# Kernel tuning notes

Hardware: AMD Instinct MI355X
Metric: run time of the kernel (lower is better)

## Reference

```python
import jax, jax.numpy as jnp
import numpy as np

C = 64
HIMG = 256
WIMG = 256
N = HIMG * WIMG
E = 8 * N
HEADS = 4
DHEAD = C // HEADS
NMOD = 9   # 9 GraphAttentionModules (c1_1..c3_3)
NLAY = 3   # layers per module
NSTACK = 2 # RBS1, RBS2
NBLK = 4   # resblocks per stack


def setup_inputs() -> dict:
    key = jax.random.key(0)
    ks = jax.random.split(key, 12)
    s = 0.05
    x = jax.random.normal(ks[0], (1, C, HIMG, WIMG), dtype=jnp.float32)
    edge_index = jax.random.randint(ks[1], (2, E), 0, N, dtype=jnp.int32)
    gat_Wl = jax.random.normal(ks[2], (NMOD, NLAY, C, C), dtype=jnp.float32) * s
    gat_Wr = jax.random.normal(ks[3], (NMOD, NLAY, C, C), dtype=jnp.float32) * s
    gat_att = jax.random.normal(ks[4], (NMOD, NLAY, HEADS, DHEAD), dtype=jnp.float32) * s
    gat_b = jax.random.normal(ks[5], (NMOD, NLAY, C), dtype=jnp.float32) * s
    cc_w = jax.random.normal(ks[6], (3, C, 3 * C), dtype=jnp.float32) * s
    cc_b = jax.random.normal(ks[7], (3, C), dtype=jnp.float32) * s
    rb_w = jax.random.normal(ks[8], (NSTACK, NBLK, 2, C, C, 3, 3), dtype=jnp.float32) * s
    rb_b = jax.random.normal(ks[9], (NSTACK, NBLK, 2, C), dtype=jnp.float32) * s
    rb_a = jnp.full((NSTACK, NBLK), 0.25, dtype=jnp.float32)  # PReLU init
    return dict(x=x, edge_index=edge_index, gat_Wl=gat_Wl, gat_Wr=gat_Wr,
                gat_att=gat_att, gat_b=gat_b, cc_w=cc_w, cc_b=cc_b,
                rb_w=rb_w, rb_b=rb_b, rb_a=rb_a)


def _gatv2(x, src, dst, Wl, Wr, att, b):
    # x: [N,C]; GATv2Conv (PyG): xl = lin_l(x) (source msgs), xr = lin_r(x) (target)
    xl = (x @ Wl).reshape(-1, HEADS, DHEAD)
    xr = (x @ Wr).reshape(-1, HEADS, DHEAD)
    xj = xl[src]                               # [E,H,D] source
    xi = xr[dst]                               # [E,H,D] target
    e = jax.nn.leaky_relu(xi + xj, 0.2)        # [E,H,D]
    logits = jnp.einsum('ehd,hd->eh', e, att)  # [E,H]
    m = jax.ops.segment_max(logits, dst, num_segments=N)
    m = jnp.where(jnp.isfinite(m), m, 0.0)
    ex = jnp.exp(logits - m[dst])
    den = jax.ops.segment_sum(ex, dst, num_segments=N)
    alpha = ex / (den[dst] + 1e-16)            # edge softmax per target node
    out = jax.ops.segment_sum(xj * alpha[..., None], dst, num_segments=N)
    return out.reshape(-1, C) + b


def _gam(xn, src, dst, m, gat_Wl, gat_Wr, gat_att, gat_b):
    # GraphAttentionModule: 3 GAT layers, each followed by ELU
    for l in range(NLAY):
        xn = jax.nn.elu(_gatv2(xn, src, dst, gat_Wl[m, l], gat_Wr[m, l],
                               gat_att[m, l], gat_b[m, l]))
    return xn


def _to_nodes(img):   # [1,C,H,W] -> [N,C]
    return img[0].transpose(1, 2, 0).reshape(N, C)


def _to_img(xn):      # [N,C] -> [1,C,H,W]
    return xn.reshape(HIMG, WIMG, C).transpose(2, 0, 1)[None]


def _conv3(x, w, b):
    y = jax.lax.conv_general_dilated(x, w, (1, 1), 'SAME',
                                     dimension_numbers=('NCHW', 'OIHW', 'NCHW'))
    return y + b[None, :, None, None]


def _resblocks(x, w, b, a):
    # stack of 4 ResBlocks: conv3 -> PReLU -> conv3, res_scale=1
    for i in range(NBLK):
        h = _conv3(x, w[i, 0], b[i, 0])
        h = jnp.where(h >= 0, h, a[i] * h)  # PReLU (single shared param)
        h = _conv3(h, w[i, 1], b[i, 1])
        x = x + h
    return x


def _stage(img, midx, ci, src, dst, gat_Wl, gat_Wr, gat_att, gat_b, cc_w, cc_b):
    xn = _to_nodes(img)
    branches = [_to_img(_gam(xn, src, dst, m, gat_Wl, gat_Wr, gat_att, gat_b))
                for m in midx]
    cat = jnp.concatenate(branches, axis=1)            # [1,3C,H,W]
    out = jnp.einsum('oc,bchw->bohw', cc_w[ci], cat) + cc_b[ci][None, :, None, None]
    return out + img


def reference(x, edge_index, gat_Wl, gat_Wr, gat_att, gat_b, cc_w, cc_b,
              rb_w, rb_b, rb_a):
    src, dst = edge_index[0], edge_index[1]
    out = _stage(x, (0, 1, 2), 0, src, dst, gat_Wl, gat_Wr, gat_att, gat_b, cc_w, cc_b)
    out = _resblocks(out, rb_w[0], rb_b[0], rb_a[0])
    out = _stage(out, (3, 4, 5), 1, src, dst, gat_Wl, gat_Wr, gat_att, gat_b, cc_w, cc_b)
    out = _resblocks(out, rb_w[1], rb_b[1], rb_a[1])
    out = _stage(out, (6, 7, 8), 2, src, dst, gat_Wl, gat_Wr, gat_att, gat_b, cc_w, cc_b)
    return out
```

## Files before the change

kernel.cpp:

```cpp
#include <hip/hip_runtime.h>
#include <hip/hip_bf16.h>
#include <math.h>

#define N_NODES 65536
#define HW      65536
#define NE      524288
#define NC      (N_NODES * 64)

typedef __bf16 bf16x8 __attribute__((ext_vector_type(8)));
typedef float  f32x4  __attribute__((ext_vector_type(4)));
typedef float  f32x2  __attribute__((ext_vector_type(2)));
typedef int    i32x4  __attribute__((ext_vector_type(4)));
typedef unsigned int uint2v __attribute__((ext_vector_type(2)));

static __device__ __forceinline__ f32x4 mfma16(bf16x8 a, bf16x8 b, f32x4 c) {
    return __builtin_amdgcn_mfma_f32_16x16x32_bf16(a, b, c, 0, 0, 0);
}

static __device__ __forceinline__ unsigned short f2bs(float f) {
    return __builtin_bit_cast(unsigned short, __float2bfloat16(f));
}

__global__ void k_hist(const int* __restrict__ dstA, int* __restrict__ cnt) {
    int e = blockIdx.x * 256 + threadIdx.x;
    if (e < NE) atomicAdd(&cnt[dstA[e]], 1);
}

__global__ void k_scan(const int* __restrict__ cnt, int* __restrict__ off) {
    __shared__ int sums[1024];
    int t = threadIdx.x;
    int base = t * 64;
    int s = 0;
    for (int i = 0; i < 64; ++i) s += cnt[base + i];
    sums[t] = s;
    __syncthreads();
    for (int d = 1; d < 1024; d <<= 1) {
        int v = (t >= d) ? sums[t - d] : 0;
        __syncthreads();
        sums[t] += v;
        __syncthreads();
    }
    int run = sums[t] - s;
    for (int i = 0; i < 64; ++i) { off[base + i] = run; run += cnt[base + i]; }
    if (t == 1023) off[N_NODES] = run;
}

__global__ void k_fill(const int* __restrict__ srcA, const int* __restrict__ dstA,
                       int* __restrict__ cur, int* __restrict__ csr) {
    int e = blockIdx.x * 256 + threadIdx.x;
    if (e < NE) {
        int p = atomicAdd(&cur[dstA[e]], 1);
        csr[p] = srcA[e];
    }
}

__global__ void k_cvpack(const float* __restrict__ w, __hip_bfloat16* __restrict__ d) {
    int idx = blockIdx.x * 256 + threadIdx.x;
    if (idx >= 589824) return;
    int j = idx & 7, lane = (idx >> 3) & 63, r = idx >> 9;
    int kk = r & 1; r >>= 1;
    int nt = r & 3; r >>= 2;
    int tap = r % 9, cv = r / 9;
    int co = nt * 16 + (lane & 15);
    int ci = kk * 32 + (lane >> 4) * 8 + j;
    d[idx] = __float2bfloat16(w[((cv * 64 + co) * 64 + ci) * 9 + tap]);
}

__global__ void k_mmpack(const float* __restrict__ Wl, const float* __restrict__ Wr,
                         __hip_bfloat16* __restrict__ d) {
    int idx = blockIdx.x * 256 + threadIdx.x;
    if (idx >= 221184) return;
    int j = idx & 7, lane = (idx >> 3) & 63, r = idx >> 9;
    int kk = r & 1; r >>= 1;
    int nt = r & 3; r >>= 2;
    int side = r & 1, lay = r >> 1;
    int co = nt * 16 + (lane & 15);
    int ci = kk * 32 + (lane >> 4) * 8 + j;
    const float* W = side ? Wr : Wl;
    d[idx] = __float2bfloat16(W[lay * 4096 + ci * 64 + co]);
}

__global__ void k_ccpack(const float* __restrict__ w, __hip_bfloat16* __restrict__ d) {
    int idx = blockIdx.x * 256 + threadIdx.x;
    if (idx >= 36864) return;
    int j = idx & 7;
    int u = idx >> 3;
    int lane = u & 63;
    int f = (u >> 6) & 7;
    int sb = u >> 9;
    int kk = f & 1, nt = f >> 1;
    int br = sb % 3, st = sb / 3;
    int k = br * 64 + kk * 32 + (lane >> 4) * 8 + j;
    int co = nt * 16 + (lane & 15);
    d[idx] = __float2bfloat16(w[st * 12288 + co * 192 + k]);
}

__global__ void k_init(const float* __restrict__ img, float* __restrict__ xn,
                       __hip_bfloat16* __restrict__ xb) {
    __shared__ float tile[64][65];
    int nb = blockIdx.x * 64;
    for (int idx = threadIdx.x; idx < 4096; idx += 256) {
        int c = idx >> 6, n = idx & 63;
        tile[c][n] = img[c * HW + nb + n];
    }
    __syncthreads();
    for (int idx = threadIdx.x; idx < 4096; idx += 256) {
        int n = idx >> 6, c = idx & 63;
        float v = tile[c][n];
        xn[(nb + n) * 64 + c] = v;
        xb[(nb + n) * 64 + c] = __float2bfloat16(v);
    }
}

static __device__ __forceinline__ void mm_phase32(char* smem, int t,
        const __hip_bfloat16* __restrict__ pwm, unsigned char* __restrict__ xlo,
        __hip_bfloat16* __restrict__ xrb, int n0) {
    i32x4* la = (i32x4*)smem;
    int lane = t & 63, side = t >> 6;
    const i32x4* wpt = (const i32x4*)pwm + side * 512 + lane;
    f32x4 acc[2][4];
#pragma unroll
    for (int mi = 0; mi < 2; ++mi)
#pragma unroll
        for (int nt = 0; nt < 4; ++nt) acc[mi][nt] = (f32x4)0.0f;
    bf16x8 b[4][2];
#pragma unroll
    for (int nt = 0; nt < 4; ++nt)
#pragma unroll
        for (int kk = 0; kk < 2; ++kk)
            b[nt][kk] = __builtin_bit_cast(bf16x8, wpt[(nt * 2 + kk) * 64]);
#pragma unroll
    for (int mi = 0; mi < 2; ++mi) {
        int row = mi * 16 + (lane & 15);
#pragma unroll
        for (int kk = 0; kk < 2; ++kk) {
            bf16x8 a = __builtin_bit_cast(bf16x8,
                la[row * 8 + (((kk << 2) | (lane >> 4)) ^ (row & 7))]);
#pragma unroll
            for (int nt = 0; nt < 4; ++nt)
                acc[mi][nt] = mfma16(a, b[nt][kk], acc[mi][nt]);
        }
    }
    __syncthreads();
    unsigned short* ls = (unsigned short*)smem;
    if (side == 0) {
#pragma unroll
        for (int mi = 0; mi < 2; ++mi)
#pragma unroll
            for (int nt = 0; nt < 4; ++nt) {
                int co = nt * 16 + (lane & 15);
#pragma unroll
                for (int r = 0; r < 4; ++r) {
                    int row = mi * 16 + (lane >> 4) * 4 + r;
                    ls[row * 68 + co] = f2bs(acc[mi][nt][r]);
                }
            }
    } else {
#pragma unroll
        for (int mi = 0; mi < 2; ++mi)
#pragma unroll
            for (int nt = 0; nt < 4; ++nt) {
                int co = nt * 16 + (lane & 15);
#pragma unroll
                for (int r = 0; r < 4; ++r) {
                    int node = n0 + mi * 16 + (lane >> 4) * 4 + r;
                    xrb[(size_t)node * 64 + co] = __float2bfloat16(acc[mi][nt][r]);
                }
            }
    }
    __syncthreads();
    for (int u = t; u < 256; u += 128) {
        int node = u >> 3, oct = u & 7;
        const unsigned short* p = ls + node * 68 + oct * 8;
        uint2v w0 = *(const uint2v*)p;
        uint2v w1 = *(const uint2v*)(p + 4);
        float f0 = __builtin_bit_cast(float, w0[0] << 16);
        float f1 = __builtin_bit_cast(float, w0[0] & 0xffff0000u);
        float f2 = __builtin_bit_cast(float, w0[1] << 16);
        float f3 = __builtin_bit_cast(float, w0[1] & 0xffff0000u);
        float f4 = __builtin_bit_cast(float, w1[0] << 16);
        float f5 = __builtin_bit_cast(float, w1[0] & 0xffff0000u);
        float f6 = __builtin_bit_cast(float, w1[1] << 16);
        float f7 = __builtin_bit_cast(float, w1[1] & 0xffff0000u);
        int v0 = 0, v1 = 0;
        v0 = __builtin_amdgcn_cvt_pk_fp8_f32(f0, f1, v0, false);
        v0 = __builtin_amdgcn_cvt_pk_fp8_f32(f2, f3, v0, true);
        v1 = __builtin_amdgcn_cvt_pk_fp8_f32(f4, f5, v1, false);
        v1 = __builtin_amdgcn_cvt_pk_fp8_f32(f6, f7, v1, true);
        uint2v o;
        o[0] = (unsigned)v0;
        o[1] = (unsigned)v1;
        *(uint2v*)(xlo + (size_t)(n0 + node) * 64 + oct * 8) = o;
    }
}

static __device__ __forceinline__ uint2v gat_node(
        const unsigned char* __restrict__ xl8, const __hip_bfloat16* __restrict__ xrb,
        const int* __restrict__ csr, const int* __restrict__ csr_c, int cbase, int cc,
        int n, int e0, int e1, int c4, f32x2 a01, f32x2 a23, f32x4 b4) {
    uint2v xw = *(const uint2v*)(xrb + (size_t)n * 64 + c4);
    f32x2 xi01, xi23;
    xi01[0] = __builtin_bit_cast(float, xw[0] << 16);
    xi01[1] = __builtin_bit_cast(float, xw[0] & 0xffff0000u);
    xi23[0] = __builtin_bit_cast(float, xw[1] << 16);
    xi23[1] = __builtin_bit_cast(float, xw[1] & 0xffff0000u);
    float s = 0.f;
    f32x2 acc01 = {0.f, 0.f}, acc23 = {0.f, 0.f};
    int rounds = (e1 - e0 + 1) >> 1;
    int e = e0;
    for (int i = 0; i < rounds; ++i, e += 2) {
        bool aB = (e + 1) < e1;
        int eB = aB ? e + 1 : e;
        int rA = e - cbase, rB = eB - cbase;
        int sA = (rA < cc) ? csr_c[rA] : csr[e];
        int sB = (rB < cc) ? csr_c[rB] : csr[eB];
        unsigned int wA = *(const unsigned int*)(xl8 + (size_t)sA * 64 + c4);
        unsigned int wB = *(const unsigned int*)(xl8 + (size_t)sB * 64 + c4);
        f32x2 xjA01 = __builtin_amdgcn_cvt_pk_f32_fp8((int)wA, false);
        f32x2 xjA23 = __builtin_amdgcn_cvt_pk_f32_fp8((int)wA, true);
        f32x2 xjB01 = __builtin_amdgcn_cvt_pk_f32_fp8((int)wB, false);
        f32x2 xjB23 = __builtin_amdgcn_cvt_pk_f32_fp8((int)wB, true);
        f32x2 vA01 = xi01 + xjA01;
        f32x2 vA23 = xi23 + xjA23;
        vA01 = __builtin_elementwise_max(vA01, vA01 * 0.2f);
        vA23 = __builtin_elementwise_max(vA23, vA23 * 0.2f);
        f32x2 pA2 = vA01 * a01 + vA23 * a23;
        float pA = pA2[0] + pA2[1];
        f32x2 vB01 = xi01 + xjB01;
        f32x2 vB23 = xi23 + xjB23;
        vB01 = __builtin_elementwise_max(vB01, vB01 * 0.2f);
        vB23 = __builtin_elementwise_max(vB23, vB23 * 0.2f);
        f32x2 pB2 = vB01 * a01 + vB23 * a23;
        float pB = pB2[0] + pB2[1];
        pA += __shfl_xor(pA, 1);
        pA += __shfl_xor(pA, 2);
        pB += __shfl_xor(pB, 1);
        pB += __shfl_xor(pB, 2);
        float exA = exp2f(fmaxf(pA, -100.f));
        float exB = exp2f(fmaxf(pB, -100.f));
        exB = aB ? exB : 0.f;
        s += exA + exB;
        acc01 = acc01 + exA * xjA01 + exB * xjB01;
        acc23 = acc23 + exA * xjA23 + exB * xjB23;
    }
    float inv = __builtin_amdgcn_rcpf(s + 1e-16f);
    float v0 = fmaf(acc01[0], inv, b4[0]);
    float v1 = fmaf(acc01[1], inv, b4[1]);
    float v2 = fmaf(acc23[0], inv, b4[2]);
    float v3 = fmaf(acc23[1], inv, b4[3]);
    v0 = v0 > 0.f ? v0 : __expf(v0) - 1.f;
    v1 = v1 > 0.f ? v1 : __expf(v1) - 1.f;
    v2 = v2 > 0.f ? v2 : __expf(v2) - 1.f;
    v3 = v3 > 0.f ? v3 : __expf(v3) - 1.f;
    uint2v o;
    o[0] = (unsigned)f2bs(v0) | ((unsigned)f2bs(v1) << 16);
    o[1] = (unsigned)f2bs(v2) | ((unsigned)f2bs(v3) << 16);
    return o;
}

__global__ __launch_bounds__(128) void k_mm3(const __hip_bfloat16* __restrict__ Xb,
        const __hip_bfloat16* __restrict__ pw, unsigned char* __restrict__ XL8,
        __hip_bfloat16* __restrict__ XRb) {
    __shared__ i32x4 smem4[272];
    char* smem = (char*)smem4;
    i32x4* la = (i32x4*)smem;
    int t = threadIdx.x;
    int m = blockIdx.x >> 11;
    int n0 = (blockIdx.x & 2047) << 5;
    const i32x4* Xg = (const i32x4*)Xb + n0 * 8;
    for (int idx = t; idx < 256; idx += 128) {
        int r = idx >> 3, c = idx & 7;
        la[r * 8 + (c ^ (r & 7))] = Xg[idx];
    }
    __syncthreads();
    mm_phase32(smem, t, pw + m * 24576, XL8 + (size_t)m * NC,
               XRb + (size_t)m * NC, n0);
}

__global__ __launch_bounds__(128) void k_fuse(
        const unsigned char* __restrict__ XL8in, unsigned char* __restrict__ XL8out,
        __hip_bfloat16* __restrict__ XRb, const float* __restrict__ gatt,
        const float* __restrict__ gb, const __hip_bfloat16* __restrict__ pw,
        const int* __restrict__ off, const int* __restrict__ csr) {
    __shared__ i32x4 smem4[272];
    __shared__ int csr_c[384];
    char* smem = (char*)smem4;
    int t = threadIdx.x;
    int p = blockIdx.x;
    int vi = (p & 7) * 768 + (p >> 3);
    int m = vi >> 11;
    int n0 = (vi & 2047) << 5;
    const unsigned char* xl8 = XL8in + (size_t)m * NC;
    unsigned char* xlo = XL8out + (size_t)m * NC;
    __hip_bfloat16* xrb = XRb + (size_t)m * NC;
    int cbase = off[n0];
    int cc = min(off[n0 + 32] - cbase, 384);
    for (int i = t; i < cc; i += 128) csr_c[i] = csr[cbase + i];
    __syncthreads();
    int g16 = t >> 4;
    int c4 = (t & 15) << 2;
    const float* at = gatt + m * 192;
    const float* bb = gb + m * 192;
    const float LOG2E = 1.44269504089f;
    f32x4 a4 = *(const f32x4*)(at + c4);
    f32x2 a01 = {a4[0] * LOG2E, a4[1] * LOG2E};
    f32x2 a23 = {a4[2] * LOG2E, a4[3] * LOG2E};
    f32x4 b4 = *(const f32x4*)(bb + c4);
    uint2v* lau = (uint2v*)smem;
    int cchunk = c4 >> 3, half = (c4 >> 2) & 1;
    for (int nn = 0; nn < 4; ++nn) {
        int r = g16 * 4 + nn;
        int n = n0 + r;
        uint2v o = gat_node(xl8, xrb, csr, csr_c, cbase, cc, n,
                            off[n], off[n + 1], c4, a01, a23, b4);
        lau[(r * 8 + (cchunk ^ (r & 7))) * 2 + half] = o;
    }
    __syncthreads();
    mm_phase32(smem, t, pw + m * 24576, xlo, xrb, n0);
}

__global__ __launch_bounds__(256) void k_gatfin(const unsigned char* __restrict__ XL8,
        const __hip_bfloat16* __restrict__ XRb, const float* __restrict__ gatt,
        const float* __restrict__ gb, const int* __restrict__ off,
        const int* __restrict__ csr, __hip_bfloat16* __restrict__ brs) {
    __shared__ int csr_c[320];
    int t = threadIdx.x, lane = t & 63;
    int p = blockIdx.x;
    int vi = (p & 7) * 768 + (p >> 3);
    int m = vi >> 11;
    int nblk = (vi & 2047) * 32;
    const unsigned char* xl8 = XL8 + (size_t)m * NC;
    const __hip_bfloat16* xrb = XRb + (size_t)m * NC;
    __hip_bfloat16* outb = brs + (size_t)m * NC;
    int cbase = off[nblk];
    int cc = min(off[nblk + 32] - cbase, 320);
    for (int i = t; i < cc; i += 256) csr_c[i] = csr[cbase + i];
    __syncthreads();
    int g = (lane >> 4) & 3;
    int c4 = (lane & 15) << 2;
    const float* at = gatt + m * 192;
    const float* bb = gb + m * 192;
    const float LOG2E = 1.44269504089f;
    f32x4 a4 = *(const f32x4*)(at + c4);
    f32x2 a01 = {a4[0] * LOG2E, a4[1] * LOG2E};
    f32x2 a23 = {a4[2] * LOG2E, a4[3] * LOG2E};
    f32x4 b4 = *(const f32x4*)(bb + c4);
    int base = nblk + ((t >> 6) << 3) + g * 2;
#pragma unroll
    for (int nn = 0; nn < 2; ++nn) {
        int n = base + nn;
        uint2v o = gat_node(xl8, xrb, csr, csr_c, cbase, cc, n,
                            off[n], off[n + 1], c4, a01, a23, b4);
        *(uint2v*)(outb + (size_t)n * 64 + c4) = o;
    }
}

__global__ __launch_bounds__(256) void k_cc2(const __hip_bfloat16* __restrict__ b0,
        const __hip_bfloat16* __restrict__ b1, const __hip_bfloat16* __restrict__ b2,
        const __hip_bfloat16* __restrict__ pw, const float* __restrict__ bias,
        const float* __restrict__ resin, float* __restrict__ imgout,
        __hip_bfloat16* __restrict__ outb) {
    __shared__ i32x4 la[128 * 8];
    int t = threadIdx.x, lane = t & 63, wid = t >> 6;
    int n0 = blockIdx.x * 128;
    const __hip_bfloat16* brs[3] = {b0, b1, b2};
    const i32x4* wp4 = (const i32x4*)pw;
    f32x4 acc[2][4];
#pragma unroll
    for (int mi = 0; mi < 2; ++mi)
#pragma unroll
        for (int nt = 0; nt < 4; ++nt) acc[mi][nt] = (f32x4)0.0f;
#pragma unroll
    for (int br = 0; br < 3; ++br) {
        __syncthreads();
        const i32x4* Bg = (const i32x4*)brs[br] + n0 * 8;
        for (int idx = t; idx < 1024; idx += 256) {
            int r = idx >> 3, c = idx & 7;
            la[r * 8 + (c ^ (r & 7))] = Bg[idx];
        }
        __syncthreads();
        bf16x8 bf[4][2];
#pragma unroll
        for (int nt = 0; nt < 4; ++nt)
#pragma unroll
            for (int kk = 0; kk < 2; ++kk)
                bf[nt][kk] = __builtin_bit_cast(bf16x8,
                    wp4[(br * 8 + nt * 2 + kk) * 64 + lane]);
#pragma unroll
        for (int mi = 0; mi < 2; ++mi) {
            int row = wid * 32 + mi * 16 + (lane & 15);
#pragma unroll
            for (int kk = 0; kk < 2; ++kk) {
                bf16x8 a = __builtin_bit_cast(bf16x8,
                    la[row * 8 + (((kk << 2) | (lane >> 4)) ^ (row & 7))]);
#pragma unroll
                for (int nt = 0; nt < 4; ++nt)
                    acc[mi][nt] = mfma16(a, bf[nt][kk], acc[mi][nt]);
            }
        }
    }
#pragma unroll
    for (int mi = 0; mi < 2; ++mi)
#pragma unroll
        for (int nt = 0; nt < 4; ++nt) {
            int co = nt * 16 + (lane & 15);
            float bv = bias[co];
#pragma unroll
            for (int r = 0; r < 4; ++r) {
                int node = n0 + wid * 32 + mi * 16 + (lane >> 4) * 4 + r;
                float v = acc[mi][nt][r] + bv + resin[node * 64 + co];
                imgout[node * 64 + co] = v;
                outb[node * 64 + co] = __float2bfloat16(v);
            }
        }
}

__global__ __launch_bounds__(256) void k_ccfin(const __hip_bfloat16* __restrict__ b0,
        const __hip_bfloat16* __restrict__ b1, const __hip_bfloat16* __restrict__ b2,
        const __hip_bfloat16* __restrict__ pw, const float* __restrict__ bias,
        const float* __restrict__ resin, float* __restrict__ outp) {
    __shared__ i32x4 la[128 * 8];
    __shared__ float tt[64][132];
    int t = threadIdx.x, lane = t & 63, wid = t >> 6;
    int n0 = blockIdx.x * 128;
    const __hip_bfloat16* brs[3] = {b0, b1, b2};
    const i32x4* wp4 = (const i32x4*)pw;
    f32x4 acc[2][4];
#pragma unroll
    for (int mi = 0; mi < 2; ++mi)
#pragma unroll
        for (int nt = 0; nt < 4; ++nt) acc[mi][nt] = (f32x4)0.0f;
#pragma unroll
    for (int br = 0; br < 3; ++br) {
        __syncthreads();
        const i32x4* Bg = (const i32x4*)brs[br] + n0 * 8;
        for (int idx = t; idx < 1024; idx += 256) {
            int r = idx >> 3, c = idx & 7;
            la[r * 8 + (c ^ (r & 7))] = Bg[idx];
        }
        __syncthreads();
        bf16x8 bf[4][2];
#pragma unroll
        for (int nt = 0; nt < 4; ++nt)
#pragma unroll
            for (int kk = 0; kk < 2; ++kk)
                bf[nt][kk] = __builtin_bit_cast(bf16x8,
                    wp4[(br * 8 + nt * 2 + kk) * 64 + lane]);
#pragma unroll
        for (int mi = 0; mi < 2; ++mi) {
            int row = wid * 32 + mi * 16 + (lane & 15);
#pragma unroll
            for (int kk = 0; kk < 2; ++kk) {
                bf16x8 a = __builtin_bit_cast(bf16x8,
                    la[row * 8 + (((kk << 2) | (lane >> 4)) ^ (row & 7))]);
#pragma unroll
                for (int nt = 0; nt < 4; ++nt)
                    acc[mi][nt] = mfma16(a, bf[nt][kk], acc[mi][nt]);
            }
        }
    }
#pragma unroll
    for (int mi = 0; mi < 2; ++mi)
#pragma unroll
        for (int nt = 0; nt < 4; ++nt) {
            int co = nt * 16 + (lane & 15);
            float bv = bias[co];
#pragma unroll
            for (int r = 0; r < 4; ++r) {
                int nl = wid * 32 + mi * 16 + (lane >> 4) * 4 + r;
                tt[co][nl] = acc[mi][nt][r] + bv + resin[(n0 + nl) * 64 + co];
            }
        }
    __syncthreads();
    for (int u = t; u < 2048; u += 256) {
        int row = u >> 5;
        int col = (u & 31) * 4;
        f32x4 v = *(const f32x4*)&tt[row][col];
        *(f32x4*)(outp + row * HW + n0 + col) = v;
    }
}

template <int MODE>
__global__ __launch_bounds__(256) void k_conv(const __hip_bfloat16* __restrict__ inb,
        const __hip_bfloat16* __restrict__ wp, const float* __restrict__ bias,
        const float* __restrict__ pa, float* __restrict__ img,
        __hip_bfloat16* __restrict__ outb) {
    __shared__ i32x4 la[2][130 * 8];
    int t = threadIdx.x, lane = t & 63, wid = t >> 6;
    int y = blockIdx.x >> 1, x0 = (blockIdx.x & 1) << 7;
    f32x4 acc[2][4];
#pragma unroll
    for (int mi = 0; mi < 2; ++mi)
#pragma unroll
        for (int nt = 0; nt < 4; ++nt) acc[mi][nt] = (f32x4)0.0f;
    const i32x4* ing = (const i32x4*)inb;
    auto stage = [&](int dy, int buf) {
        int sy = y + dy - 1;
        bool rowok = (sy >= 0) && (sy < 256);
        for (int idx = t; idx < 1040; idx += 256) {
            int r = idx >> 3, c = idx & 7;
            int sx = x0 - 1 + r;
            i32x4 v = (i32x4)0;
            if (rowok && sx >= 0 && sx < 256) v = ing[(sy * 256 + sx) * 8 + c];
            la[buf][r * 8 + (c ^ (r & 7))] = v;
        }
    };
    stage(0, 0);
    __syncthreads();
#pragma unroll
    for (int dy = 0; dy < 3; ++dy) {
        if (dy < 2) stage(dy + 1, (dy + 1) & 1);
        const i32x4* lb = la[dy & 1];
#pragma unroll
        for (int dx = 0; dx < 3; ++dx) {
            const i32x4* wpt = (const i32x4*)wp + (dy * 3 + dx) * 512 + lane;
            bf16x8 b[4][2];
#pragma unroll
            for (int nt = 0; nt < 4; ++nt)
#pragma unroll
                for (int kk = 0; kk < 2; ++kk)
                    b[nt][kk] = __builtin_bit_cast(bf16x8, wpt[(nt * 2 + kk) * 64]);
#pragma unroll
            for (int mi = 0; mi < 2; ++mi) {
                int row = dx + wid * 32 + mi * 16 + (lane & 15);
#pragma unroll
                for (int kk = 0; kk < 2; ++kk) {
                    bf16x8 a = __builtin_bit_cast(bf16x8,
                        lb[row * 8 + (((kk << 2) | (lane >> 4)) ^ (row & 7))]);
#pragma unroll
                    for (int nt = 0; nt < 4; ++nt)
                        acc[mi][nt] = mfma16(a, b[nt][kk], acc[mi][nt]);
                }
            }
        }
        __syncthreads();
    }
    int pbase = y * 256 + x0 + wid * 32 + (lane >> 4) * 4;
    float aprelu = (MODE == 0) ? pa[0] : 0.f;
#pragma unroll
    for (int mi = 0; mi < 2; ++mi)
#pragma unroll
        for (int nt = 0; nt < 4; ++nt) {
            int co = nt * 16 + (lane & 15);
            float bv = bias[co];
#pragma unroll
            for (int r = 0; r < 4; ++r) {
                int pix = pbase + mi * 16 + r;
                float v = acc[mi][nt][r] + bv;
                if (MODE == 0) {
                    v = v >= 0.f ? v : aprelu * v;
                    outb[pix * 64 + co] = __float2bfloat16(v);
                } else {
                    v += img[pix * 64 + co];
                    img[pix * 64 + co] = v;
                    outb[pix * 64 + co] = __float2bfloat16(v);
                }
            }
        }
}

extern "C" void kernel_launch(void* const* d_in, const int* in_sizes, int n_in,
                              void* d_out, int out_size, void* d_ws, size_t ws_size,
                              hipStream_t stream) {
    const float* x    = (const float*)d_in[0];
    const int*   ei   = (const int*)d_in[1];
    const float* gWl  = (const float*)d_in[2];
    const float* gWr  = (const float*)d_in[3];
    const float* gatt = (const float*)d_in[4];
    const float* gb   = (const float*)d_in[5];
    const float* ccw  = (const float*)d_in[6];
    const float* ccb  = (const float*)d_in[7];
    const float* rbw  = (const float*)d_in[8];
    const float* rbb  = (const float*)d_in[9];
    const float* rba  = (const float*)d_in[10];
    float* outp = (float*)d_out;

    float* wsf = (float*)d_ws;
    float* xn  = wsf;
    float* img = xn + NC;
    __hip_bfloat16* xrb3 = (__hip_bfloat16*)(img + NC);
    unsigned char* xl8p0 = (unsigned char*)(xrb3 + 3 * (size_t)NC);
    unsigned char* xl8p1 = xl8p0 + 3 * (size_t)NC;
    __hip_bfloat16* xb   = (__hip_bfloat16*)(xl8p1 + 3 * (size_t)NC);
    __hip_bfloat16* b0b  = xb + NC;
    __hip_bfloat16* b1b  = b0b + NC;
    __hip_bfloat16* b2b  = b1b + NC;
    __hip_bfloat16* cvb  = b0b;
    __hip_bfloat16* wpkc = b2b + NC;
    __hip_bfloat16* wpkm = wpkc + 589824;
    __hip_bfloat16* ccpk = wpkm + 221184;
    int* ioff = (int*)(ccpk + 36864);
    int* icnt = ioff + (N_NODES + 1);
    int* icur = icnt + N_NODES;
    int* icsr = icur + N_NODES;

    const int* srcA = ei;
    const int* dstA = ei + NE;

    hipMemsetAsync(icnt, 0, N_NODES * sizeof(int), stream);
    k_hist<<<NE / 256, 256, 0, stream>>>(dstA, icnt);
    k_scan<<<1, 1024, 0, stream>>>(icnt, ioff);
    hipMemcpyAsync(icur, ioff, N_NODES * sizeof(int), hipMemcpyDeviceToDevice, stream);
    k_fill<<<NE / 256, 256, 0, stream>>>(srcA, dstA, icur, icsr);
    k_cvpack<<<2304, 256, 0, stream>>>(rbw, wpkc);
    k_mmpack<<<864, 256, 0, stream>>>(gWl, gWr, wpkm);
    k_ccpack<<<144, 256, 0, stream>>>(ccw, ccpk);
    k_init<<<1024, 256, 0, stream>>>(x, xn, xb);

    for (int st = 0; st < 3; ++st) {
        int L = st * 9;
        k_mm3<<<6144, 128, 0, stream>>>(xb, wpkm + (size_t)L * 8192, xl8p0, xrb3);
        k_fuse<<<6144, 128, 0, stream>>>(xl8p0, xl8p1, xrb3,
            gatt + L * 64, gb + L * 64, wpkm + (size_t)(L + 1) * 8192, ioff, icsr);
        k_fuse<<<6144, 128, 0, stream>>>(xl8p1, xl8p0, xrb3,
            gatt + (L + 1) * 64, gb + (L + 1) * 64, wpkm + (size_t)(L + 2) * 8192,
            ioff, icsr);
        k_gatfin<<<6144, 256, 0, stream>>>(xl8p0, xrb3,
            gatt + (L + 2) * 64, gb + (L + 2) * 64, ioff, icsr, b0b);
        const float* resin = (st == 0) ? xn : img;
        if (st == 2) {
            k_ccfin<<<N_NODES / 128, 256, 0, stream>>>(b0b, b1b, b2b,
                ccpk + 2 * 12288, ccb + 128, resin, outp);
        } else {
            k_cc2<<<N_NODES / 128, 256, 0, stream>>>(b0b, b1b, b2b,
                ccpk + st * 12288, ccb + st * 64, resin, img, xb);
            for (int bk = 0; bk < 4; ++bk) {
                int cv = (st * 4 + bk) * 2;
                k_conv<0><<<512, 256, 0, stream>>>(xb, wpkc + (size_t)cv * 36864,
                    rbb + cv * 64, rba + st * 4 + bk, nullptr, cvb);
                k_conv<1><<<512, 256, 0, stream>>>(cvb, wpkc + (size_t)(cv + 1) * 36864,
                    rbb + (cv + 1) * 64, nullptr, img, xb);
            }
        }
    }
}
```

Measured before the change: 0.9996 ms.

## Degree-sort nodes within blocks for GAT balance and halve conv tile width

A new setup kernel sorts the 32 nodes of each block by in-degree. The fused GAT kernels then assign nodes to thread groups in a snake order over that ranking, so each group gets a similar total edge count and the wave waits less on its slowest group. Separately, the 3x3 conv kernel now covers 64 pixels per block instead of 128 (1024 blocks instead of 512), which reduces per-thread accumulators and raises the number of blocks in flight. The cost is more halo reloads in the conv and an extra indirection load per node in the GAT kernels.

Measured after the change: 971.3 us. 2.8% less time.

```diff
diff --git a/kernel.cpp b/kernel.cpp
--- a/kernel.cpp
+++ b/kernel.cpp
@@ -52,6 +52,29 @@
         int p = atomicAdd(&cur[dstA[e]], 1);
         csr[p] = srcA[e];
     }
+}
+
+__global__ void k_bsort(const int* __restrict__ off, int* __restrict__ bperm) {
+    int b = blockIdx.x * 256 + threadIdx.x;
+    if (b >= 2048) return;
+    int base = b * 32;
+    int deg[32], idx[32];
+#pragma unroll
+    for (int i = 0; i < 32; ++i) {
+        deg[i] = off[base + i + 1] - off[base + i];
+        idx[i] = i;
+    }
+    for (int i = 1; i < 32; ++i) {
+        int d = deg[i], x = idx[i], j = i - 1;
+        while (j >= 0 && deg[j] < d) {
+            deg[j + 1] = deg[j];
+            idx[j + 1] = idx[j];
+            --j;
+        }
+        deg[j + 1] = d;
+        idx[j + 1] = x;
+    }
+    for (int i = 0; i < 32; ++i) bperm[base + i] = idx[i];
 }
 
 __global__ void k_cvpack(const float* __restrict__ w, __hip_bfloat16* __restrict__ d) {
@@ -281,7 +304,8 @@
         const unsigned char* __restrict__ XL8in, unsigned char* __restrict__ XL8out,
         __hip_bfloat16* __restrict__ XRb, const float* __restrict__ gatt,
         const float* __restrict__ gb, const __hip_bfloat16* __restrict__ pw,
-        const int* __restrict__ off, const int* __restrict__ csr) {
+        const int* __restrict__ off, const int* __restrict__ csr,
+        const int* __restrict__ bperm) {
     __shared__ i32x4 smem4[272];
     __shared__ int csr_c[384];
     char* smem = (char*)smem4;
@@ -308,8 +332,11 @@
     f32x4 b4 = *(const f32x4*)(bb + c4);
     uint2v* lau = (uint2v*)smem;
     int cchunk = c4 >> 3, half = (c4 >> 2) & 1;
+    const int* bp = bperm + n0;
+#pragma unroll
     for (int nn = 0; nn < 4; ++nn) {
-        int r = g16 * 4 + nn;
+        int rank = (nn & 1) ? (nn * 8 + (7 - g16)) : (nn * 8 + g16);
+        int r = bp[rank];
         int n = n0 + r;
         uint2v o = gat_node(xl8, xrb, csr, csr_c, cbase, cc, n,
                             off[n], off[n + 1], c4, a01, a23, b4);
@@ -322,7 +349,8 @@
 __global__ __launch_bounds__(256) void k_gatfin(const unsigned char* __restrict__ XL8,
         const __hip_bfloat16* __restrict__ XRb, const float* __restrict__ gatt,
         const float* __restrict__ gb, const int* __restrict__ off,
-        const int* __restrict__ csr, __hip_bfloat16* __restrict__ brs) {
+        const int* __restrict__ csr, __hip_bfloat16* __restrict__ brs,
+        const int* __restrict__ bperm) {
     __shared__ int csr_c[320];
     int t = threadIdx.x, lane = t & 63;
     int p = blockIdx.x;
@@ -337,6 +365,7 @@
     for (int i = t; i < cc; i += 256) csr_c[i] = csr[cbase + i];
     __syncthreads();
     int g = (lane >> 4) & 3;
+    int gg = (t >> 6) * 4 + g;
     int c4 = (lane & 15) << 2;
     const float* at = gatt + m * 192;
     const float* bb = gb + m * 192;
@@ -345,10 +374,11 @@
     f32x2 a01 = {a4[0] * LOG2E, a4[1] * LOG2E};
     f32x2 a23 = {a4[2] * LOG2E, a4[3] * LOG2E};
     f32x4 b4 = *(const f32x4*)(bb + c4);
-    int base = nblk + ((t >> 6) << 3) + g * 2;
+    const int* bp = bperm + nblk;
 #pragma unroll
     for (int nn = 0; nn < 2; ++nn) {
-        int n = base + nn;
+        int rank = (nn & 1) ? (16 + (15 - gg)) : gg;
+        int n = nblk + bp[rank];
         uint2v o = gat_node(xl8, xrb, csr, csr_c, cbase, cc, n,
                             off[n], off[n + 1], c4, a01, a23, b4);
         *(uint2v*)(outb + (size_t)n * 64 + c4) = o;
@@ -485,19 +515,17 @@
         const __hip_bfloat16* __restrict__ wp, const float* __restrict__ bias,
         const float* __restrict__ pa, float* __restrict__ img,
         __hip_bfloat16* __restrict__ outb) {
-    __shared__ i32x4 la[2][130 * 8];
+    __shared__ i32x4 la[2][66 * 8];
     int t = threadIdx.x, lane = t & 63, wid = t >> 6;
-    int y = blockIdx.x >> 1, x0 = (blockIdx.x & 1) << 7;
-    f32x4 acc[2][4];
-#pragma unroll
-    for (int mi = 0; mi < 2; ++mi)
-#pragma unroll
-        for (int nt = 0; nt < 4; ++nt) acc[mi][nt] = (f32x4)0.0f;
+    int y = blockIdx.x >> 2, x0 = (blockIdx.x & 3) << 6;
+    f32x4 acc[4];
+#pragma unroll
+    for (int nt = 0; nt < 4; ++nt) acc[nt] = (f32x4)0.0f;
     const i32x4* ing = (const i32x4*)inb;
     auto stage = [&](int dy, int buf) {
         int sy = y + dy - 1;
         bool rowok = (sy >= 0) && (sy < 256);
-        for (int idx = t; idx < 1040; idx += 256) {
+        for (int idx = t; idx < 528; idx += 256) {
             int r = idx >> 3, c = idx & 7;
             int sx = x0 - 1 + r;
             i32x4 v = (i32x4)0;
@@ -520,43 +548,38 @@
 #pragma unroll
                 for (int kk = 0; kk < 2; ++kk)
                     b[nt][kk] = __builtin_bit_cast(bf16x8, wpt[(nt * 2 + kk) * 64]);
-#pragma unroll
-            for (int mi = 0; mi < 2; ++mi) {
-                int row = dx + wid * 32 + mi * 16 + (lane & 15);
-#pragma unroll
-                for (int kk = 0; kk < 2; ++kk) {
-                    bf16x8 a = __builtin_bit_cast(bf16x8,
-                        lb[row * 8 + (((kk << 2) | (lane >> 4)) ^ (row & 7))]);
-#pragma unroll
-                    for (int nt = 0; nt < 4; ++nt)
-                        acc[mi][nt] = mfma16(a, b[nt][kk], acc[mi][nt]);
-                }
+            int row = dx + wid * 16 + (lane & 15);
+#pragma unroll
+            for (int kk = 0; kk < 2; ++kk) {
+                bf16x8 a = __builtin_bit_cast(bf16x8,
+                    lb[row * 8 + (((kk << 2) | (lane >> 4)) ^ (row & 7))]);
+#pragma unroll
+                for (int nt = 0; nt < 4; ++nt)
+                    acc[nt] = mfma16(a, b[nt][kk], acc[nt]);
             }
         }
         __syncthreads();
     }
-    int pbase = y * 256 + x0 + wid * 32 + (lane >> 4) * 4;
+    int pbase = y * 256 + x0 + wid * 16 + (lane >> 4) * 4;
     float aprelu = (MODE == 0) ? pa[0] : 0.f;
 #pragma unroll
-    for (int mi = 0; mi < 2; ++mi)
-#pragma unroll
-        for (int nt = 0; nt < 4; ++nt) {
-            int co = nt * 16 + (lane & 15);
-            float bv = bias[co];
-#pragma unroll
-            for (int r = 0; r < 4; ++r) {
-                int pix = pbase + mi * 16 + r;
-                float v = acc[mi][nt][r] + bv;
-                if (MODE == 0) {
-                    v = v >= 0.f ? v : aprelu * v;
-                    outb[pix * 64 + co] = __float2bfloat16(v);
-                } else {
-                    v += img[pix * 64 + co];
-                    img[pix * 64 + co] = v;
-                    outb[pix * 64 + co] = __float2bfloat16(v);
-                }
-            }
-        }
+    for (int nt = 0; nt < 4; ++nt) {
+        int co = nt * 16 + (lane & 15);
+        float bv = bias[co];
+#pragma unroll
+        for (int r = 0; r < 4; ++r) {
+            int pix = pbase + r;
+            float v = acc[nt][r] + bv;
+            if (MODE == 0) {
+                v = v >= 0.f ? v : aprelu * v;
+                outb[pix * 64 + co] = __float2bfloat16(v);
+            } else {
+                v += img[pix * 64 + co];
+                img[pix * 64 + co] = v;
+                outb[pix * 64 + co] = __float2bfloat16(v);
+            }
+        }
+    }
 }
 
 extern "C" void kernel_launch(void* const* d_in, const int* in_sizes, int n_in,
@@ -593,6 +616,7 @@
     int* icnt = ioff + (N_NODES + 1);
     int* icur = icnt + N_NODES;
     int* icsr = icur + N_NODES;
+    int* ibperm = icsr + NE;
 
     const int* srcA = ei;
     const int* dstA = ei + NE;
@@ -602,6 +626,7 @@
     k_scan<<<1, 1024, 0, stream>>>(icnt, ioff);
     hipMemcpyAsync(icur, ioff, N_NODES * sizeof(int), hipMemcpyDeviceToDevice, stream);
     k_fill<<<NE / 256, 256, 0, stream>>>(srcA, dstA, icur, icsr);
+    k_bsort<<<8, 256, 0, stream>>>(ioff, ibperm);
     k_cvpack<<<2304, 256, 0, stream>>>(rbw, wpkc);
     k_mmpack<<<864, 256, 0, stream>>>(gWl, gWr, wpkm);
     k_ccpack<<<144, 256, 0, stream>>>(ccw, ccpk);
@@ -611,12 +636,13 @@
         int L = st * 9;
         k_mm3<<<6144, 128, 0, stream>>>(xb, wpkm + (size_t)L * 8192, xl8p0, xrb3);
         k_fuse<<<6144, 128, 0, stream>>>(xl8p0, xl8p1, xrb3,
-            gatt + L * 64, gb + L * 64, wpkm + (size_t)(L + 1) * 8192, ioff, icsr);
+            gatt + L * 64, gb + L * 64, wpkm + (size_t)(L + 1) * 8192, ioff, icsr,
+            ibperm);
         k_fuse<<<6144, 128, 0, stream>>>(xl8p1, xl8p0, xrb3,
             gatt + (L + 1) * 64, gb + (L + 1) * 64, wpkm + (size_t)(L + 2) * 8192,
-            ioff, icsr);
+            ioff, icsr, ibperm);
         k_gatfin<<<6144, 256, 0, stream>>>(xl8p0, xrb3,
-            gatt + (L + 2) * 64, gb + (L + 2) * 64, ioff, icsr, b0b);
+            gatt + (L + 2) * 64, gb + (L + 2) * 64, ioff, icsr, b0b, ibperm);
         const float* resin = (st == 0) ? xn : img;
         if (st == 2) {
             k_ccfin<<<N_NODES / 128, 256, 0, stream>>>(b0b, b1b, b2b,
@@ -626,9 +652,9 @@
                 ccpk + st * 12288, ccb + st * 64, resin, img, xb);
             for (int bk = 0; bk < 4; ++bk) {
                 int cv = (st * 4 + bk) * 2;
-                k_conv<0><<<512, 256, 0, stream>>>(xb, wpkc + (size_t)cv * 36864,
+                k_conv<0><<<1024, 256, 0, stream>>>(xb, wpkc + (size_t)cv * 36864,
                     rbb + cv * 64, rba + st * 4 + bk, nullptr, cvb);
-                k_conv<1><<<512, 256, 0, stream>>>(cvb, wpkc + (size_t)(cv + 1) * 36864,
+                k_conv<1><<<1024, 256, 0, stream>>>(cvb, wpkc + (size_t)(cv + 1) * 36864,
                     rbb + (cv + 1) * 64, nullptr, img, xb);
             }
         }
```
